# Kernel tuning notes

Hardware: AMD Instinct MI355X
Metric: run time of the kernel (lower is better)

Reference implementation:

```python
import jax, jax.numpy as jnp
import numpy as np

N = 100000  # nodes
E = 1600000  # edges
F = 128      # nfeat == nclass (source constructs every layer as nfeat->nclass)


def setup_inputs() -> dict:
    key = jax.random.key(0)
    ks = jax.random.split(key, 8)
    x = jax.random.normal(ks[0], (N, F), dtype=jnp.float32)
    row = jax.random.randint(ks[1], (E,), 0, N)
    col = jax.random.randint(ks[2], (E,), 0, N)
    s = (1.0 / np.sqrt(F)).astype(np.float32) if hasattr(1.0/np.sqrt(F), 'astype') else 1.0/np.sqrt(F)
    s = 1.0 / np.sqrt(F)
    W0 = jax.random.uniform(ks[3], (F, F), jnp.float32, -s, s)
    b0 = jax.random.uniform(ks[4], (F,), jnp.float32, -s, s)
    W1 = jax.random.uniform(ks[5], (F, F), jnp.float32, -s, s)
    b1 = jax.random.uniform(ks[6], (F,), jnp.float32, -s, s)
    return {"x": x, "W0": W0, "b0": b0, "W1": W1, "b1": b1, "row": row, "col": col}


def _gcn_layer(h_in, W, b, row, col, dinv):
    # h = Linear(feat)
    h = h_in @ W + b
    # (D^-1/2 (A+I) D^-1/2) @ h, A in COO (row=i, col=j), A[i,j]=1
    coef = dinv[row] * dinv[col]                      # [E]
    msg = h[col] * coef[:, None]                       # [E, F] gather
    agg = jax.ops.segment_sum(msg, row, num_segments=N)
    agg = agg + (dinv * dinv)[:, None] * h             # self loops (identity)
    return agg


def reference(x, W0, b0, W1, b1, row, col):
    # D_hat = diag((A + I).sum(0)) -> column sums + 1
    deg = jax.ops.segment_sum(jnp.ones((E,), jnp.float32), col, num_segments=N) + 1.0
    dinv = deg ** -0.5
    h = _gcn_layer(x, W0, b0, row, col, dinv)
    h = jax.nn.relu(h)            # with_relu=True; dropout off (eval mode)
    h = _gcn_layer(h, W1, b1, row, col, dinv)
    return jax.nn.log_softmax(h, axis=1)
```

## Files before the change

kernel.cpp:

```cpp
#include <hip/hip_runtime.h>
#include <math.h>

#define FDIM 128
#define RPB 256
#define BSTRIDE 32
#define NBLK 512
#define MAXB 512
#define NSUB 8
#define SCAP 1024
#define CAP (NSUB * SCAP)

typedef __attribute__((ext_vector_type(8))) short short8;
typedef __attribute__((ext_vector_type(4))) float floatx4;

static __device__ __forceinline__ unsigned short f2bf(float f) {
    unsigned int u = __float_as_uint(f);
    u = (u + 0x7fff + ((u >> 16) & 1)) >> 16;
    return (unsigned short)u;
}

static __device__ __forceinline__ unsigned int cvtpk(float a, float b) {
    unsigned int r;
    asm("v_cvt_pk_bf16_f32 %0, %1, %2" : "=v"(r) : "v"(a), "v"(b));
    return r;
}

static __device__ __forceinline__ void bf2f(unsigned int u, float& a, float& b) {
    a = __uint_as_float(u << 16);
    b = __uint_as_float(u & 0xffff0000u);
}


__global__ __launch_bounds__(256) void k_init(int* rbCnt, int* cbCnt, int nb, unsigned int* hsz,
                                              float* dinvN,
                                              const float* __restrict__ W0, const float* __restrict__ W1,
                                              unsigned short* __restrict__ W0t, unsigned short* __restrict__ W1t) {
    const int b = blockIdx.x;
    const int tid = threadIdx.x;
    if (b >= 2) {
        int i0 = (b - 2) * 256 + tid;
        int tot = nb * NSUB;
        for (int i = i0; i < tot; i += (gridDim.x - 2) * 256) {
            rbCnt[(size_t)i * BSTRIDE] = 0;
            cbCnt[(size_t)i * BSTRIDE] = 0;
        }
        if (b == 2 && tid < 64) hsz[tid] = 0u;
        if (b == 2 && tid == 64) *dinvN = 0.0f;
    } else {
        const float* W = (b == 0) ? W0 : W1;
        unsigned short* Wt = (b == 0) ? W0t : W1t;
        for (int idx = tid; idx < FDIM * FDIM; idx += 256) {
            int k = idx >> 7, c = idx & 127;
            Wt[c * FDIM + k] = f2bf(W[idx]);
        }
    }
}


#define KH 64
#define LPAD 72
#define GSMEM (2 * 128 * LPAD * 2)

static __device__ __forceinline__ void gemm_body(char* smem, const void* __restrict__ Ain,
                                                 const unsigned short* __restrict__ Wt,
                                                 const float* __restrict__ bias,
                                                 const float* __restrict__ dinv,
                                                 unsigned int* __restrict__ outp, int n,
                                                 int af32, int scaled, int blk) {
    unsigned short (*sA)[LPAD] = (unsigned short(*)[LPAD])smem;
    unsigned short (*sW)[LPAD] = (unsigned short(*)[LPAD])(smem + 128 * LPAD * 2);

    const unsigned short* A = (const unsigned short*)Ain;
    const float* Af = (const float*)Ain;

    const int tid = threadIdx.x;
    const int row0 = blk * 128;
    const int wid = tid >> 6;
    const int lane = tid & 63;
    const int quad = lane >> 4;
    const int lq = lane & 15;
    const int wm = wid & 1;
    const int wn = wid >> 1;

    floatx4 acc[4][4];
#pragma unroll
    for (int i = 0; i < 4; i++)
#pragma unroll
        for (int j = 0; j < 4; j++) acc[i][j] = (floatx4){0.f, 0.f, 0.f, 0.f};

    for (int kh = 0; kh < 2; kh++) {
        if (kh) __syncthreads();
#pragma unroll
        for (int it = 0; it < 4; it++) {
            int f = tid + it * 256;
            int r = f >> 3;
            int c8 = (f & 7) * 8;
            int gr = row0 + r;
            if (af32) {
                float4 v0 = make_float4(0.f, 0.f, 0.f, 0.f);
                float4 v1 = make_float4(0.f, 0.f, 0.f, 0.f);
                if (gr < n) {
                    v0 = *(const float4*)&Af[(size_t)gr * FDIM + kh * KH + c8];
                    v1 = *(const float4*)&Af[(size_t)gr * FDIM + kh * KH + c8 + 4];
                }
                uint4 p;
                p.x = cvtpk(v0.x, v0.y);
                p.y = cvtpk(v0.z, v0.w);
                p.z = cvtpk(v1.x, v1.y);
                p.w = cvtpk(v1.z, v1.w);
                *(uint4*)&sA[r][c8] = p;
            } else {
                uint4 v = make_uint4(0u, 0u, 0u, 0u);
                if (gr < n) v = *(const uint4*)&A[(size_t)gr * FDIM + kh * KH + c8];
                *(uint4*)&sA[r][c8] = v;
            }
            uint4 wv = *(const uint4*)&Wt[(size_t)r * FDIM + kh * KH + c8];
            *(uint4*)&sW[r][c8] = wv;
        }
        __syncthreads();

#pragma unroll
        for (int kt = 0; kt < 2; kt++) {
            const int k0 = kt * 32 + quad * 8;
            short8 af[4], bf[4];
#pragma unroll
            for (int mt = 0; mt < 4; mt++)
                af[mt] = *(const short8*)&sA[wm * 64 + mt * 16 + lq][k0];
#pragma unroll
            for (int nt = 0; nt < 4; nt++)
                bf[nt] = *(const short8*)&sW[wn * 64 + nt * 16 + lq][k0];
#pragma unroll
            for (int mt = 0; mt < 4; mt++)
#pragma unroll
                for (int nt = 0; nt < 4; nt++)
                    acc[mt][nt] = __builtin_amdgcn_mfma_f32_16x16x32_bf16(af[mt], bf[nt], acc[mt][nt], 0, 0, 0);
        }
    }

    float bv[4];
#pragma unroll
    for (int nt = 0; nt < 4; nt++) bv[nt] = bias[wn * 64 + nt * 16 + lq];

#pragma unroll
    for (int mt = 0; mt < 4; mt++) {
#pragma unroll
        for (int r = 0; r < 4; r++) {
            int grow = row0 + wm * 64 + mt * 16 + quad * 4 + r;
            float di = scaled ? ((grow < n) ? dinv[grow] : 0.f) : 1.0f;
#pragma unroll
            for (int nt = 0; nt < 4; nt++) {
                float v = (acc[mt][nt][r] + bv[nt]) * di;
                float pv = __shfl_xor(v, 1, 64);
                if (!(lq & 1) && grow < n) {
                    int col = wn * 64 + nt * 16 + lq;
                    outp[(size_t)grow * 64 + (col >> 1)] =
                        (unsigned int)f2bf(v) | ((unsigned int)f2bf(pv) << 16);
                }
            }
        }
    }
}


__global__ __launch_bounds__(256) void k_scatter_gemm(const int* __restrict__ row, const int* __restrict__ col,
                                                      int* rbCnt, int* cbCnt,
                                                      unsigned int* __restrict__ pairs,
                                                      unsigned char* __restrict__ clocal, int nE, int nb,
                                                      const float* __restrict__ x,
                                                      const unsigned short* __restrict__ W0t,
                                                      const float* __restrict__ b0,
                                                      unsigned int* __restrict__ hs, int n) {
    __shared__ __align__(16) char smem[GSMEM];

    if (blockIdx.x >= NBLK) {
        gemm_body(smem, (const void*)x, W0t, b0, (const float*)nullptr, hs, n, 1, 0, blockIdx.x - NBLK);
        return;
    }

    int* rh    = (int*)smem;
    int* ch    = (int*)(smem + MAXB * 4);
    int* rbase = (int*)(smem + MAXB * 8);
    int* cbase = (int*)(smem + MAXB * 12);
    const int tid = threadIdx.x;
    const int sub = blockIdx.x & (NSUB - 1);
    const int cpb = (nE + NBLK - 1) / NBLK;
    const int e0 = blockIdx.x * cpb;
    int e1 = e0 + cpb; if (e1 > nE) e1 = nE;

    for (int i = tid; i < nb; i += 256) { rh[i] = 0; ch[i] = 0; }
    __syncthreads();
    for (int e = e0 + tid; e < e1; e += 256) {
        atomicAdd(&rh[row[e] >> 8], 1);
        atomicAdd(&ch[col[e] >> 8], 1);
    }
    __syncthreads();
    for (int i = tid; i < nb; i += 256) {
        rbase[i] = rh[i] ? (i * CAP + sub * SCAP +
                            atomicAdd(&rbCnt[(size_t)(i * NSUB + sub) * BSTRIDE], rh[i])) : 0;
        cbase[i] = ch[i] ? (i * CAP + sub * SCAP +
                            atomicAdd(&cbCnt[(size_t)(i * NSUB + sub) * BSTRIDE], ch[i])) : 0;
        rh[i] = 0;
        ch[i] = 0;
    }
    __syncthreads();
    const int pmax = nb * CAP - 1;
    for (int e = e0 + tid; e < e1; e += 256) {
        int r = row[e];
        int c = col[e];
        int rb = r >> 8, cb = c >> 8;
        int p = rbase[rb] + atomicAdd(&rh[rb], 1);
        if (p > pmax) p = pmax;
        pairs[p] = ((unsigned int)(r & (RPB - 1)) << 24) | (unsigned int)c;
        int q = cbase[cb] + atomicAdd(&ch[cb], 1);
        if (q > pmax) q = pmax;
        clocal[q] = (unsigned char)(c & (RPB - 1));
    }
}


__global__ __launch_bounds__(512) void k_sortdinv(const int* __restrict__ rbCnt, const int* __restrict__ cbCnt,
                                                  const unsigned int* __restrict__ pairs,
                                                  const unsigned char* __restrict__ clocal,
                                                  uint2* __restrict__ rse, float* __restrict__ dinv,
                                                  int* __restrict__ csr_col, int n, int nb) {
    __shared__ int chist[RPB];
    __shared__ int hist[RPB];
    __shared__ int scan[RPB];
    __shared__ int lcur[RPB];
    const int b = blockIdx.x;
    const int tid = threadIdx.x;
    const int grp = tid >> 8;
    const int lt = tid & 255;
    const int row0 = b * RPB;
    const int base4 = lt * 4;

    if (tid < RPB) { hist[tid] = 0; chist[tid] = 0; }
    __syncthreads();

#pragma unroll
    for (int sp = 0; sp < NSUB; sp += 2) {
        const int s = sp + grp;
        int rc = rbCnt[(size_t)(b * NSUB + s) * BSTRIDE]; if (rc > SCAP) rc = SCAP;
        int cc = cbCnt[(size_t)(b * NSUB + s) * BSTRIDE]; if (cc > SCAP) cc = SCAP;
        const unsigned int* seg = &pairs[(size_t)b * CAP + s * SCAP];
        if (base4 < rc) {
            uint4 v = *(const uint4*)&seg[base4];
            atomicAdd(&hist[v.x >> 24], 1);
            if (base4 + 1 < rc) atomicAdd(&hist[v.y >> 24], 1);
            if (base4 + 2 < rc) atomicAdd(&hist[v.z >> 24], 1);
            if (base4 + 3 < rc) atomicAdd(&hist[v.w >> 24], 1);
        }
        const unsigned int* cseg = (const unsigned int*)&clocal[(size_t)b * CAP + s * SCAP];
        if (base4 < cc) {
            unsigned int cv = cseg[lt];
            atomicAdd(&chist[cv & 255], 1);
            if (base4 + 1 < cc) atomicAdd(&chist[(cv >> 8) & 255], 1);
            if (base4 + 2 < cc) atomicAdd(&chist[(cv >> 16) & 255], 1);
            if (base4 + 3 < cc) atomicAdd(&chist[cv >> 24], 1);
        }
    }
    __syncthreads();

    if (tid < RPB) scan[tid] = hist[tid];
    __syncthreads();
    for (int off = 1; off < RPB; off <<= 1) {
        int t = (tid < RPB && tid >= off) ? scan[tid - off] : 0;
        __syncthreads();
        if (tid < RPB) scan[tid] += t;
        __syncthreads();
    }
    if (tid < RPB) {
        int ex = b * CAP + scan[tid] - hist[tid];
        lcur[tid] = ex;
        int r = row0 + tid;
        if (r < n) {
            rse[r] = make_uint2((unsigned int)ex, (unsigned int)(ex + hist[tid]));
            dinv[r] = rsqrtf((float)chist[tid] + 1.0f);
        }
    }
    __syncthreads();

#pragma unroll
    for (int sp = 0; sp < NSUB; sp += 2) {
        const int s = sp + grp;
        int rc = rbCnt[(size_t)(b * NSUB + s) * BSTRIDE]; if (rc > SCAP) rc = SCAP;
        const unsigned int* seg = &pairs[(size_t)b * CAP + s * SCAP];
        if (base4 < rc) {
            uint4 v = *(const uint4*)&seg[base4];
            int pos = atomicAdd(&lcur[v.x >> 24], 1);
            csr_col[pos] = (int)(v.x & 0x00FFFFFFu);
            if (base4 + 1 < rc) { pos = atomicAdd(&lcur[v.y >> 24], 1); csr_col[pos] = (int)(v.y & 0x00FFFFFFu); }
            if (base4 + 2 < rc) { pos = atomicAdd(&lcur[v.z >> 24], 1); csr_col[pos] = (int)(v.z & 0x00FFFFFFu); }
            if (base4 + 3 < rc) { pos = atomicAdd(&lcur[v.w >> 24], 1); csr_col[pos] = (int)(v.w & 0x00FFFFFFu); }
        }
    }
}


__global__ __launch_bounds__(256) void k_gemm_mfma(const void* __restrict__ Ain,
                                                   const unsigned short* __restrict__ Wt,
                                                   const float* __restrict__ bias,
                                                   const float* __restrict__ dinv,
                                                   unsigned int* __restrict__ outp, int n, int af32) {
    __shared__ __align__(16) char smem[GSMEM];
    gemm_body(smem, Ain, Wt, bias, dinv, outp, n, af32, 1, blockIdx.x);
}


#define UACC(U) { float p_, q_; \
    bf2f(U.x, p_, q_); acc0 += p_; acc1 += q_; \
    bf2f(U.y, p_, q_); acc2 += p_; acc3 += q_; \
    bf2f(U.z, p_, q_); acc4 += p_; acc5 += q_; \
    bf2f(U.w, p_, q_); acc6 += p_; acc7 += q_; }

#define UACCD(U, DJ) { float p_, q_; \
    bf2f(U.x, p_, q_); acc0 = fmaf(p_, DJ, acc0); acc1 = fmaf(q_, DJ, acc1); \
    bf2f(U.y, p_, q_); acc2 = fmaf(p_, DJ, acc2); acc3 = fmaf(q_, DJ, acc3); \
    bf2f(U.z, p_, q_); acc4 = fmaf(p_, DJ, acc4); acc5 = fmaf(q_, DJ, acc5); \
    bf2f(U.w, p_, q_); acc6 = fmaf(p_, DJ, acc6); acc7 = fmaf(q_, DJ, acc7); }

__global__ __launch_bounds__(256) void k_agg0(const unsigned int* __restrict__ hs,
                                              const uint2* __restrict__ rse,
                                              const int* __restrict__ csr_col, const float* __restrict__ dinv,
                                              unsigned int* __restrict__ out, int n) {
    int w = (blockIdx.x * 256 + threadIdx.x) >> 6;
    int lane = threadIdx.x & 63;
    if (w >= n) return;
    const int quad = lane >> 4;
    const int lq = lane & 15;

    const uint2 se = rse[w];
    int e = (int)se.x;
    const int end = (int)se.y;
    const float di = dinv[w];

    uint4 sv = make_uint4(0u, 0u, 0u, 0u);
    if (quad == 0) sv = *(const uint4*)&hs[(size_t)w * 64 + lq * 4];
    float acc0, acc1, acc2, acc3, acc4, acc5, acc6, acc7;
    bf2f(sv.x, acc0, acc1);
    bf2f(sv.y, acc2, acc3);
    bf2f(sv.z, acc4, acc5);
    bf2f(sv.w, acc6, acc7);
    acc0 *= di; acc1 *= di; acc2 *= di; acc3 *= di;
    acc4 *= di; acc5 *= di; acc6 *= di; acc7 *= di;

    const int zrow = n;

    while (e < end) {
        int cnt = end - e;
        if (cnt > 64) cnt = 64;
        int jv = (e + lane < end) ? csr_col[e + lane] : zrow;
        int nb8 = (cnt + 7) >> 3;
        for (int t = 0; t < nb8; t++) {
            int i0 = t * 8 + quad;
            int j0 = __shfl(jv, i0, 64);
            int j1 = __shfl(jv, i0 + 4, 64);
            uint4 u0 = *(const uint4*)&hs[(size_t)j0 * 64 + lq * 4];
            uint4 u1 = *(const uint4*)&hs[(size_t)j1 * 64 + lq * 4];
            float dj0 = dinv[j0];
            float dj1 = dinv[j1];
            UACCD(u0, dj0)
            UACCD(u1, dj1)
        }
        e += cnt;
    }

    acc0 += __shfl_xor(acc0, 16, 64); acc0 += __shfl_xor(acc0, 32, 64);
    acc1 += __shfl_xor(acc1, 16, 64); acc1 += __shfl_xor(acc1, 32, 64);
    acc2 += __shfl_xor(acc2, 16, 64); acc2 += __shfl_xor(acc2, 32, 64);
    acc3 += __shfl_xor(acc3, 16, 64); acc3 += __shfl_xor(acc3, 32, 64);
    acc4 += __shfl_xor(acc4, 16, 64); acc4 += __shfl_xor(acc4, 32, 64);
    acc5 += __shfl_xor(acc5, 16, 64); acc5 += __shfl_xor(acc5, 32, 64);
    acc6 += __shfl_xor(acc6, 16, 64); acc6 += __shfl_xor(acc6, 32, 64);
    acc7 += __shfl_xor(acc7, 16, 64); acc7 += __shfl_xor(acc7, 32, 64);

    acc0 *= di; acc1 *= di; acc2 *= di; acc3 *= di;
    acc4 *= di; acc5 *= di; acc6 *= di; acc7 *= di;
    acc0 = fmaxf(acc0, 0.f); acc1 = fmaxf(acc1, 0.f);
    acc2 = fmaxf(acc2, 0.f); acc3 = fmaxf(acc3, 0.f);
    acc4 = fmaxf(acc4, 0.f); acc5 = fmaxf(acc5, 0.f);
    acc6 = fmaxf(acc6, 0.f); acc7 = fmaxf(acc7, 0.f);

    if (quad == 0) {
        uint4 o;
        o.x = (unsigned int)f2bf(acc0) | ((unsigned int)f2bf(acc1) << 16);
        o.y = (unsigned int)f2bf(acc2) | ((unsigned int)f2bf(acc3) << 16);
        o.z = (unsigned int)f2bf(acc4) | ((unsigned int)f2bf(acc5) << 16);
        o.w = (unsigned int)f2bf(acc6) | ((unsigned int)f2bf(acc7) << 16);
        *(uint4*)&out[(size_t)w * 64 + lq * 4] = o;
    }
}

__global__ __launch_bounds__(256) void k_agg1(const unsigned int* __restrict__ hs,
                                              const uint2* __restrict__ rse,
                                              const int* __restrict__ csr_col, const float* __restrict__ dinv,
                                              float* __restrict__ out, int n) {
    int w = (blockIdx.x * 256 + threadIdx.x) >> 6;
    int lane = threadIdx.x & 63;
    if (w >= n) return;
    const int quad = lane >> 4;
    const int lq = lane & 15;

    const uint2 se = rse[w];
    int e = (int)se.x;
    const int end = (int)se.y;
    const float di = dinv[w];

    uint4 sv = make_uint4(0u, 0u, 0u, 0u);
    if (quad == 0) sv = *(const uint4*)&hs[(size_t)w * 64 + lq * 4];
    float acc0, acc1, acc2, acc3, acc4, acc5, acc6, acc7;
    bf2f(sv.x, acc0, acc1);
    bf2f(sv.y, acc2, acc3);
    bf2f(sv.z, acc4, acc5);
    bf2f(sv.w, acc6, acc7);

    const int zrow = n;

    while (e < end) {
        int cnt = end - e;
        if (cnt > 64) cnt = 64;
        int jv = (e + lane < end) ? csr_col[e + lane] : zrow;
        int nb8 = (cnt + 7) >> 3;
        for (int t = 0; t < nb8; t++) {
            int i0 = t * 8 + quad;
            int j0 = __shfl(jv, i0, 64);
            int j1 = __shfl(jv, i0 + 4, 64);
            uint4 u0 = *(const uint4*)&hs[(size_t)j0 * 64 + lq * 4];
            uint4 u1 = *(const uint4*)&hs[(size_t)j1 * 64 + lq * 4];
            UACC(u0)
            UACC(u1)
        }
        e += cnt;
    }

    acc0 += __shfl_xor(acc0, 16, 64); acc0 += __shfl_xor(acc0, 32, 64);
    acc1 += __shfl_xor(acc1, 16, 64); acc1 += __shfl_xor(acc1, 32, 64);
    acc2 += __shfl_xor(acc2, 16, 64); acc2 += __shfl_xor(acc2, 32, 64);
    acc3 += __shfl_xor(acc3, 16, 64); acc3 += __shfl_xor(acc3, 32, 64);
    acc4 += __shfl_xor(acc4, 16, 64); acc4 += __shfl_xor(acc4, 32, 64);
    acc5 += __shfl_xor(acc5, 16, 64); acc5 += __shfl_xor(acc5, 32, 64);
    acc6 += __shfl_xor(acc6, 16, 64); acc6 += __shfl_xor(acc6, 32, 64);
    acc7 += __shfl_xor(acc7, 16, 64); acc7 += __shfl_xor(acc7, 32, 64);

    acc0 *= di; acc1 *= di; acc2 *= di; acc3 *= di;
    acc4 *= di; acc5 *= di; acc6 *= di; acc7 *= di;

    float m = fmaxf(fmaxf(fmaxf(acc0, acc1), fmaxf(acc2, acc3)),
                    fmaxf(fmaxf(acc4, acc5), fmaxf(acc6, acc7)));
#pragma unroll
    for (int off = 1; off < 16; off <<= 1) m = fmaxf(m, __shfl_xor(m, off, 64));
    float s = ((expf(acc0 - m) + expf(acc1 - m)) + (expf(acc2 - m) + expf(acc3 - m))) +
              ((expf(acc4 - m) + expf(acc5 - m)) + (expf(acc6 - m) + expf(acc7 - m)));
#pragma unroll
    for (int off = 1; off < 16; off <<= 1) s += __shfl_xor(s, off, 64);
    float lg = m + logf(s);
    acc0 -= lg; acc1 -= lg; acc2 -= lg; acc3 -= lg;
    acc4 -= lg; acc5 -= lg; acc6 -= lg; acc7 -= lg;

    if (quad < 2) {
        float4 o = quad ? make_float4(acc4, acc5, acc6, acc7)
                        : make_float4(acc0, acc1, acc2, acc3);
        *(float4*)&out[(size_t)w * 128 + lq * 8 + quad * 4] = o;
    }
}


extern "C" void kernel_launch(void* const* d_in, const int* in_sizes, int n_in,
                              void* d_out, int out_size, void* d_ws, size_t ws_size,
                              hipStream_t stream) {
    const float* x  = (const float*)d_in[0];
    const float* W0 = (const float*)d_in[1];
    const float* b0 = (const float*)d_in[2];
    const float* W1 = (const float*)d_in[3];
    const float* b1 = (const float*)d_in[4];
    const int* row  = (const int*)d_in[5];
    const int* col  = (const int*)d_in[6];
    float* out = (float*)d_out;

    const int N = in_sizes[0] / FDIM;
    const int E = in_sizes[5];
    const int NB = (N + RPB - 1) / RPB;

    char* w = (char*)d_ws;
    size_t off = 0;
    auto alloc = [&](size_t bytes) {
        char* p = w + off;
        off += (bytes + 255) & ~(size_t)255;
        return p;
    };
    int* rbCnt   = (int*)alloc((size_t)NB * NSUB * BSTRIDE * 4);
    int* cbCnt   = (int*)alloc((size_t)NB * NSUB * BSTRIDE * 4);
    float* dinv  = (float*)alloc((size_t)(N + 1) * 4);
    uint2* rse   = (uint2*)alloc((size_t)N * 8);
    int* csr_col = (int*)alloc((size_t)NB * CAP * 4);
    unsigned short* W0t = (unsigned short*)alloc((size_t)FDIM * FDIM * 2);
    unsigned short* W1t = (unsigned short*)alloc((size_t)FDIM * FDIM * 2);
    unsigned int* hs = (unsigned int*)alloc((size_t)(N + 1) * 64 * 4);
    size_t pairsSz = (size_t)NB * CAP * 4;
    size_t clocSz  = (size_t)NB * CAP;
    size_t uniSz   = pairsSz + clocSz + 512;
    size_t hbSz    = (size_t)N * 64 * 4;
    char* uni = (char*)alloc(uniSz > hbSz ? uniSz : hbSz);
    unsigned int* pairs = (unsigned int*)uni;
    unsigned char* clocal = (unsigned char*)(uni + pairsSz);
    unsigned int* hb = (unsigned int*)uni;

    const int gW = (N * 64 + 255) / 256;
    const int gG = (N + 127) / 128;

    k_init<<<16, 256, 0, stream>>>(rbCnt, cbCnt, NB, hs + (size_t)N * 64, dinv + N, W0, W1, W0t, W1t);
    k_scatter_gemm<<<NBLK + gG, 256, 0, stream>>>(row, col, rbCnt, cbCnt, pairs, clocal, E, NB,
                                                  x, W0t, b0, hs, N);
    k_sortdinv<<<NB, 512, 0, stream>>>(rbCnt, cbCnt, pairs, clocal, rse, dinv, csr_col, N, NB);

    k_agg0<<<gW, 256, 0, stream>>>(hs, rse, csr_col, dinv, hb, N);

    k_gemm_mfma<<<gG, 256, 0, stream>>>((const void*)hb, W1t, b1, dinv, hs, N, 0);
    k_agg1<<<gW, 256, 0, stream>>>(hs, rse, csr_col, dinv, out, N);
}
```

Before: 338.0 us.

## Split edge bucketing into two-pass coarse/fine radix scatter

Replaces the single-pass edge scatter into 391 row/col buckets with two passes. A coarse kernel first partitions edges into 8 groups by bucket index modulo 8, and a fine kernel then splits each group into at most 64 buckets. Each pass uses a small shared histogram and writes to fewer, more contiguous destinations, aiming for better write coalescing and less contention on shared atomics. In exchange it adds a kernel launch and an extra round trip through memory for the intermediate arrays (8-byte row/col pairs plus 4-byte cols). It also relies on a fixed capacity per subgroup.

Measured after the change: 339.6 us. About the same (+0.5%).

```diff
diff --git a/kernel.cpp b/kernel.cpp
--- a/kernel.cpp
+++ b/kernel.cpp
@@ -4,12 +4,17 @@
 #define FDIM 128
 #define RPB 256
 #define BSTRIDE 32
-#define NBLK 512
 #define MAXB 512
 #define NSUB 8
 #define SCAP 1024
 #define CAP (NSUB * SCAP)
 
+#define NBLK_A 2048
+#define NGRP 8
+#define SGCAP 27520
+#define GCAP (NGRP * SGCAP)
+#define NFBLK 1024
+
 typedef __attribute__((ext_vector_type(8))) short short8;
 typedef __attribute__((ext_vector_type(4))) float floatx4;
 
@@ -31,8 +36,8 @@
 }
 
 
-__global__ __launch_bounds__(256) void k_init(int* rbCnt, int* cbCnt, int nb, unsigned int* hsz,
-                                              float* dinvN,
+__global__ __launch_bounds__(256) void k_init(int* rbCnt, int* cbCnt, int* rgCnt, int* cgCnt,
+                                              int nb, unsigned int* hsz, float* dinvN,
                                               const float* __restrict__ W0, const float* __restrict__ W1,
                                               unsigned short* __restrict__ W0t, unsigned short* __restrict__ W1t) {
     const int b = blockIdx.x;
@@ -44,8 +49,10 @@
             rbCnt[(size_t)i * BSTRIDE] = 0;
             cbCnt[(size_t)i * BSTRIDE] = 0;
         }
-        if (b == 2 && tid < 64) hsz[tid] = 0u;
-        if (b == 2 && tid == 64) *dinvN = 0.0f;
+        if (b == 2) {
+            if (tid < 64) { hsz[tid] = 0u; rgCnt[tid * BSTRIDE] = 0; cgCnt[tid * BSTRIDE] = 0; }
+            if (tid == 64) *dinvN = 0.0f;
+        }
     } else {
         const float* W = (b == 0) ? W0 : W1;
         unsigned short* Wt = (b == 0) ? W0t : W1t;
@@ -53,6 +60,49 @@
             int k = idx >> 7, c = idx & 127;
             Wt[c * FDIM + k] = f2bf(W[idx]);
         }
+    }
+}
+
+
+__global__ __launch_bounds__(256) void k_coarse(const int* __restrict__ row, const int* __restrict__ col,
+                                                int* rgCnt, int* cgCnt,
+                                                uint2* __restrict__ rowsA, unsigned int* __restrict__ colsA,
+                                                int nE) {
+    __shared__ int rc8[NGRP], cc8[NGRP], rb8[NGRP], cb8[NGRP];
+    const int tid = threadIdx.x;
+    const int sub = blockIdx.x & 7;
+    const int cpb = (nE + NBLK_A - 1) / NBLK_A;
+    const int e0 = blockIdx.x * cpb;
+    int e1 = e0 + cpb; if (e1 > nE) e1 = nE;
+
+    if (tid < NGRP) { rc8[tid] = 0; cc8[tid] = 0; }
+    __syncthreads();
+    for (int e = e0 + tid; e < e1; e += 256) {
+        atomicAdd(&rc8[(row[e] >> 8) & 7], 1);
+        atomicAdd(&cc8[(col[e] >> 8) & 7], 1);
+    }
+    __syncthreads();
+    if (tid < NGRP) {
+        int c = rc8[tid];
+        rb8[tid] = c ? (tid * GCAP + sub * SGCAP + atomicAdd(&rgCnt[(tid * 8 + sub) * BSTRIDE], c)) : 0;
+        rc8[tid] = 0;
+        c = cc8[tid];
+        cb8[tid] = c ? (tid * GCAP + sub * SGCAP + atomicAdd(&cgCnt[(tid * 8 + sub) * BSTRIDE], c)) : 0;
+        cc8[tid] = 0;
+    }
+    __syncthreads();
+    const int amax = NGRP * GCAP - 1;
+    for (int e = e0 + tid; e < e1; e += 256) {
+        int r = row[e];
+        int c = col[e];
+        int gr = (r >> 8) & 7;
+        int gc = (c >> 8) & 7;
+        int p = rb8[gr] + atomicAdd(&rc8[gr], 1);
+        if (p > amax) p = amax;
+        rowsA[p] = make_uint2((unsigned int)r, (unsigned int)c);
+        int q = cb8[gc] + atomicAdd(&cc8[gc], 1);
+        if (q > amax) q = amax;
+        colsA[q] = (unsigned int)c;
     }
 }
 
@@ -162,58 +212,79 @@
 }
 
 
-__global__ __launch_bounds__(256) void k_scatter_gemm(const int* __restrict__ row, const int* __restrict__ col,
-                                                      int* rbCnt, int* cbCnt,
-                                                      unsigned int* __restrict__ pairs,
-                                                      unsigned char* __restrict__ clocal, int nE, int nb,
-                                                      const float* __restrict__ x,
-                                                      const unsigned short* __restrict__ W0t,
-                                                      const float* __restrict__ b0,
-                                                      unsigned int* __restrict__ hs, int n) {
+__global__ __launch_bounds__(256) void k_fine_gemm(const int* __restrict__ rgCnt, const int* __restrict__ cgCnt,
+                                                   const uint2* __restrict__ rowsA,
+                                                   const unsigned int* __restrict__ colsA,
+                                                   int* rbCnt, int* cbCnt,
+                                                   unsigned int* __restrict__ pairs,
+                                                   unsigned char* __restrict__ clocal, int nb,
+                                                   const float* __restrict__ x,
+                                                   const unsigned short* __restrict__ W0t,
+                                                   const float* __restrict__ b0,
+                                                   unsigned int* __restrict__ hs, int n) {
     __shared__ __align__(16) char smem[GSMEM];
-
-    if (blockIdx.x >= NBLK) {
-        gemm_body(smem, (const void*)x, W0t, b0, (const float*)nullptr, hs, n, 1, 0, blockIdx.x - NBLK);
+    const int bi = blockIdx.x;
+    if (bi >= NFBLK) {
+        gemm_body(smem, (const void*)x, W0t, b0, (const float*)nullptr, hs, n, 1, 0, bi - NFBLK);
         return;
     }
 
-    int* rh    = (int*)smem;
-    int* ch    = (int*)(smem + MAXB * 4);
-    int* rbase = (int*)(smem + MAXB * 8);
-    int* cbase = (int*)(smem + MAXB * 12);
+    int* fh    = (int*)smem;
+    int* fbase = (int*)smem + 64;
     const int tid = threadIdx.x;
-    const int sub = blockIdx.x & (NSUB - 1);
-    const int cpb = (nE + NBLK - 1) / NBLK;
-    const int e0 = blockIdx.x * cpb;
-    int e1 = e0 + cpb; if (e1 > nE) e1 = nE;
-
-    for (int i = tid; i < nb; i += 256) { rh[i] = 0; ch[i] = 0; }
-    __syncthreads();
-    for (int e = e0 + tid; e < e1; e += 256) {
-        atomicAdd(&rh[row[e] >> 8], 1);
-        atomicAdd(&ch[col[e] >> 8], 1);
-    }
-    __syncthreads();
-    for (int i = tid; i < nb; i += 256) {
-        rbase[i] = rh[i] ? (i * CAP + sub * SCAP +
-                            atomicAdd(&rbCnt[(size_t)(i * NSUB + sub) * BSTRIDE], rh[i])) : 0;
-        cbase[i] = ch[i] ? (i * CAP + sub * SCAP +
-                            atomicAdd(&cbCnt[(size_t)(i * NSUB + sub) * BSTRIDE], ch[i])) : 0;
-        rh[i] = 0;
-        ch[i] = 0;
+    const int rside = (bi < 512);
+    const int b2 = bi & 511;
+    const int g = b2 >> 6;
+    const int j = b2 & 63;
+    const int s_src = j >> 3;
+    const int q = j & 7;
+
+    const int* gc = rside ? rgCnt : cgCnt;
+    int T = gc[(g * 8 + s_src) * BSTRIDE];
+    if (T > SGCAP) T = SGCAP;
+    const int per = (T + 7) >> 3;
+    const int sbase = g * GCAP + s_src * SGCAP;
+    int e0 = sbase + q * per;
+    int e1 = e0 + per;
+    int eend = sbase + T;
+    if (e1 > eend) e1 = eend;
+
+    if (tid < 64) fh[tid] = 0;
+    __syncthreads();
+    if (rside) {
+        for (int e = e0 + tid; e < e1; e += 256)
+            atomicAdd(&fh[rowsA[e].x >> 11], 1);
+    } else {
+        for (int e = e0 + tid; e < e1; e += 256)
+            atomicAdd(&fh[colsA[e] >> 11], 1);
+    }
+    __syncthreads();
+    int* bcnt = rside ? rbCnt : cbCnt;
+    if (tid < 64) {
+        int b = tid * 8 + g;
+        int c = fh[tid];
+        fbase[tid] = (c && b < nb) ? (b * CAP + q * SCAP +
+                        atomicAdd(&bcnt[(size_t)(b * NSUB + q) * BSTRIDE], c)) : 0;
+        fh[tid] = 0;
     }
     __syncthreads();
     const int pmax = nb * CAP - 1;
-    for (int e = e0 + tid; e < e1; e += 256) {
-        int r = row[e];
-        int c = col[e];
-        int rb = r >> 8, cb = c >> 8;
-        int p = rbase[rb] + atomicAdd(&rh[rb], 1);
-        if (p > pmax) p = pmax;
-        pairs[p] = ((unsigned int)(r & (RPB - 1)) << 24) | (unsigned int)c;
-        int q = cbase[cb] + atomicAdd(&ch[cb], 1);
-        if (q > pmax) q = pmax;
-        clocal[q] = (unsigned char)(c & (RPB - 1));
+    if (rside) {
+        for (int e = e0 + tid; e < e1; e += 256) {
+            uint2 rc = rowsA[e];
+            int fb = rc.x >> 11;
+            int p = fbase[fb] + atomicAdd(&fh[fb], 1);
+            if (p > pmax) p = pmax;
+            pairs[p] = ((rc.x & 255u) << 24) | rc.y;
+        }
+    } else {
+        for (int e = e0 + tid; e < e1; e += 256) {
+            unsigned int c = colsA[e];
+            int fb = c >> 11;
+            int p = fbase[fb] + atomicAdd(&fh[fb], 1);
+            if (p > pmax) p = pmax;
+            clocal[p] = (unsigned char)(c & 255u);
+        }
     }
 }
 
@@ -490,27 +561,34 @@
     };
     int* rbCnt   = (int*)alloc((size_t)NB * NSUB * BSTRIDE * 4);
     int* cbCnt   = (int*)alloc((size_t)NB * NSUB * BSTRIDE * 4);
+    int* rgCnt   = (int*)alloc((size_t)64 * BSTRIDE * 4);
+    int* cgCnt   = (int*)alloc((size_t)64 * BSTRIDE * 4);
     float* dinv  = (float*)alloc((size_t)(N + 1) * 4);
     uint2* rse   = (uint2*)alloc((size_t)N * 8);
     int* csr_col = (int*)alloc((size_t)NB * CAP * 4);
     unsigned short* W0t = (unsigned short*)alloc((size_t)FDIM * FDIM * 2);
     unsigned short* W1t = (unsigned short*)alloc((size_t)FDIM * FDIM * 2);
     unsigned int* hs = (unsigned int*)alloc((size_t)(N + 1) * 64 * 4);
-    size_t pairsSz = (size_t)NB * CAP * 4;
-    size_t clocSz  = (size_t)NB * CAP;
-    size_t uniSz   = pairsSz + clocSz + 512;
+    size_t rowsASz = (size_t)NGRP * GCAP * 8;
+    size_t colsASz = (size_t)NGRP * GCAP * 4;
     size_t hbSz    = (size_t)N * 64 * 4;
-    char* uni = (char*)alloc(uniSz > hbSz ? uniSz : hbSz);
-    unsigned int* pairs = (unsigned int*)uni;
-    unsigned char* clocal = (unsigned char*)(uni + pairsSz);
-    unsigned int* hb = (unsigned int*)uni;
+    size_t uni1Sz  = rowsASz + colsASz;
+    if (hbSz > uni1Sz) uni1Sz = hbSz;
+    char* uni1 = (char*)alloc(uni1Sz);
+    uint2* rowsA = (uint2*)uni1;
+    unsigned int* colsA = (unsigned int*)(uni1 + rowsASz);
+    unsigned int* hb = (unsigned int*)uni1;
+    unsigned int* pairs = (unsigned int*)alloc((size_t)NB * CAP * 4);
+    unsigned char* clocal = (unsigned char*)alloc((size_t)NB * CAP);
 
     const int gW = (N * 64 + 255) / 256;
     const int gG = (N + 127) / 128;
 
-    k_init<<<16, 256, 0, stream>>>(rbCnt, cbCnt, NB, hs + (size_t)N * 64, dinv + N, W0, W1, W0t, W1t);
-    k_scatter_gemm<<<NBLK + gG, 256, 0, stream>>>(row, col, rbCnt, cbCnt, pairs, clocal, E, NB,
-                                                  x, W0t, b0, hs, N);
+    k_init<<<16, 256, 0, stream>>>(rbCnt, cbCnt, rgCnt, cgCnt, NB, hs + (size_t)N * 64, dinv + N,
+                                   W0, W1, W0t, W1t);
+    k_coarse<<<NBLK_A, 256, 0, stream>>>(row, col, rgCnt, cgCnt, rowsA, colsA, E);
+    k_fine_gemm<<<NFBLK + gG, 256, 0, stream>>>(rgCnt, cgCnt, rowsA, colsA, rbCnt, cbCnt,
+                                                pairs, clocal, NB, x, W0t, b0, hs, N);
     k_sortdinv<<<NB, 512, 0, stream>>>(rbCnt, cbCnt, pairs, clocal, rse, dinv, csr_col, N, NB);
 
     k_agg0<<<gW, 256, 0, stream>>>(hs, rse, csr_col, dinv, hb, N);
```
